# Optimization experiments

Hardware: AMD Instinct MI355X
Metric: run time of the kernel (lower is better)

## Reference

```python
import jax, jax.numpy as jnp
import numpy as np

IN_F, OUT_F, R = 4096, 4096, 16
SCALING = 32.0 / R  # lora_alpha / r


def setup_inputs() -> dict:
    key = jax.random.key(0)
    kx, kw, kb, ka, kB = jax.random.split(key, 5)
    bound_w = 1.0 / np.sqrt(IN_F)  # kaiming_uniform a=sqrt(5) on (out,in) -> U(-1/sqrt(in), 1/sqrt(in))
    x = jax.random.normal(kx, (4, 4096, IN_F), dtype=jnp.float32)
    weight = jax.random.uniform(kw, (OUT_F, IN_F), jnp.float32, -bound_w, bound_w)
    bias = jax.random.uniform(kb, (OUT_F,), jnp.float32, -bound_w, bound_w)
    lora_A = jax.random.uniform(ka, (R, IN_F), jnp.float32, -bound_w, bound_w)
    # B is zero-init in the module; use small random values so the LoRA path is exercised
    lora_B = jax.random.normal(kB, (OUT_F, R), dtype=jnp.float32) * 0.01
    return {"x": x, "weight": weight, "bias": bias, "lora_A": lora_A, "lora_B": lora_B}


def reference(x, weight, bias, lora_A, lora_B):
    # base: F.linear(x, W, b) = x @ W.T + b
    base_out = jnp.einsum("bsi,oi->bso", x, weight) + bias
    # low-rank path: (x @ A.T) @ B.T * scaling  (dropout=0 -> identity)
    xr = jnp.einsum("bsi,ri->bsr", x, lora_A)  # [b, s, r]
    lora_out = jnp.einsum("bsr,or->bso", xr, lora_B) * SCALING
    return base_out + lora_out
```

## Files before the change

### kernel.cpp

```cpp
#include <hip/hip_runtime.h>
#include <hip/hip_bf16.h>


typedef __attribute__((ext_vector_type(8))) short bf16x8;
typedef __attribute__((ext_vector_type(16))) float f32x16;
typedef __attribute__((ext_vector_type(4))) unsigned short u16x4;

#define M_DIM 16384
#define N_DIM 4096
#define K_DIM 4096
#define NT 64

__device__ __forceinline__ unsigned short f2bf(float f) {
    unsigned int u = __builtin_bit_cast(unsigned int, f);
    unsigned int r = u + 0x7FFFu + ((u >> 16) & 1u);
    return (unsigned short)(r >> 16);
}

__device__ __forceinline__ void async16(const void* g, void* l) {
    __builtin_amdgcn_global_load_lds(
        (const __attribute__((address_space(1))) unsigned int*)g,
        (__attribute__((address_space(3))) unsigned int*)l,
        16, 0, 0);
}

__global__ void __launch_bounds__(256) cast_x_kernel(
    const float* __restrict__ x, unsigned short* __restrict__ y) {
    const int total = 512 * 256 * 64;
    int idx = blockIdx.x * 256 + threadIdx.x;
    const int stride = gridDim.x * 256;
    for (; idx < total; idx += stride) {
        const int frag = idx >> 6, l = idx & 63;
        const int m = ((frag >> 8) << 5) + (l & 31);
        const int k = ((frag & 255) << 4) + ((l >> 5) << 3);
        const float4* px = reinterpret_cast<const float4*>(&x[(size_t)m * K_DIM + k]);
        float4 a = px[0], b = px[1];
        unsigned short r[8] = { f2bf(a.x), f2bf(a.y), f2bf(a.z), f2bf(a.w),
                                f2bf(b.x), f2bf(b.y), f2bf(b.z), f2bf(b.w) };
        *reinterpret_cast<bf16x8*>(&y[((size_t)frag << 9) + (l << 3)]) =
            *reinterpret_cast<const bf16x8*>(r);
    }
}

__global__ void __launch_bounds__(256) weff_kernel(
    const float* __restrict__ W, const float* __restrict__ lA,
    const float* __restrict__ lB, unsigned short* __restrict__ out) {
    constexpr int K = K_DIM, R = 16;
    constexpr float S = 2.0f;
    int o = blockIdx.x;
    int t = threadIdx.x;
    float b[R];
#pragma unroll
    for (int r = 0; r < R; ++r) b[r] = lB[o * R + r];
#pragma unroll
    for (int c = 0; c < 4; ++c) {
        int i = c * 1024 + t * 4;
        float4 wv = *reinterpret_cast<const float4*>(&W[o * K + i]);
        float sx = 0.f, sy = 0.f, sz = 0.f, sw = 0.f;
#pragma unroll
        for (int r = 0; r < R; ++r) {
            float4 a = *reinterpret_cast<const float4*>(&lA[r * K + i]);
            sx += b[r] * a.x; sy += b[r] * a.y;
            sz += b[r] * a.z; sw += b[r] * a.w;
        }
        u16x4 ov = { f2bf(wv.x + S * sx), f2bf(wv.y + S * sy),
                     f2bf(wv.z + S * sz), f2bf(wv.w + S * sw) };
        const int frag = (o >> 5) * 256 + (i >> 4);
        const int lane_ = (o & 31) + (((i >> 3) & 1) << 5);
        *reinterpret_cast<u16x4*>(
            &out[((size_t)frag << 9) + (lane_ << 3) + (i & 7)]) = ov;
    }
}

#define ASTAGE(t, bsel, jlo, jhi)                                             \
    _Pragma("unroll") for (int j = (jlo); j <= (jhi); ++j) {                  \
        const int g = wid * 4 + j;                                            \
        async16(A + (((size_t)(bm * 8 + (g >> 2)) * 256 + (t) * 4 + (g & 3))  \
                     << 9) + (lane << 3),                                     \
                lds + (bsel) * 65536 + g * 1024 + (lane << 4));               \
    }

#define BSTAGE(t, bsel)                                                       \
    _Pragma("unroll") for (int j = 0; j < 4; ++j) {                           \
        const int g = wid * 4 + j;                                            \
        async16(B + (((size_t)(bn * 8 + (g >> 2)) * 256 + (t) * 4 + (g & 3))  \
                     << 9) + (lane << 3),                                     \
                lds + (bsel) * 65536 + 32768 + g * 1024 + (lane << 4));       \
    }

#define LDA32(dst, mh, kh, bsel)                                              \
    _Pragma("unroll") for (int mm = 0; mm < 2; ++mm)                          \
    _Pragma("unroll") for (int kk = 0; kk < 2; ++kk)                          \
        dst[mm * 2 + kk] = *(const bf16x8*)(lds + (bsel) * 65536 +            \
            (((wm * 4 + (mh) * 2 + mm) * 4 + (kh) * 2 + kk) << 10) +          \
            (lane << 4));

#define LDB32(dst, kh, bsel)                                                  \
    _Pragma("unroll") for (int nn = 0; nn < 2; ++nn)                          \
    _Pragma("unroll") for (int kk = 0; kk < 2; ++kk)                          \
        dst[nn * 2 + kk] = *(const bf16x8*)(lds + (bsel) * 65536 + 32768 +    \
            (((wn * 2 + nn) * 4 + (kh) * 2 + kk) << 10) + (lane << 4));

#define MMQ(asrc, bsrc, mh)                                                   \
    __builtin_amdgcn_s_setprio(1);                                            \
    _Pragma("unroll") for (int kk = 0; kk < 2; ++kk)                          \
    _Pragma("unroll") for (int mm = 0; mm < 2; ++mm)                          \
    _Pragma("unroll") for (int nn = 0; nn < 2; ++nn)                          \
        acc[(mh) * 2 + mm][nn] = __builtin_amdgcn_mfma_f32_32x32x16_bf16(     \
            asrc[mm * 2 + kk], bsrc[nn * 2 + kk], acc[(mh) * 2 + mm][nn],     \
            0, 0, 0);                                                         \
    __builtin_amdgcn_s_setprio(0)

#define CFENCE() asm volatile("" ::: "memory")
#define WAIT_LGKM(n)                                                          \
    asm volatile("s_waitcnt lgkmcnt(" #n ")" ::: "memory");                   \
    __builtin_amdgcn_sched_barrier(0)

#define KTILE(t)                                                              \
    {                                                                         \
        const int bs_ = (t) & 1, bo_ = bs_ ^ 1;                               \
        LDA32(arE, 0, 0, bs_);                                    \
        LDB32(br0, 0, bs_);                                       \
        if ((t) + 1 < NT) ASTAGE((t) + 1, bo_, 0, 1);                         \
        LDA32(arO, 1, 0, bs_);                                     \
        WAIT_LGKM(4);                                                         \
        MMQ(arE, br0, 0);                                                     \
        if ((t) + 1 < NT) ASTAGE((t) + 1, bo_, 2, 3);                         \
        LDA32(arE2, 0, 1, bs_);                                   \
        LDB32(br1, 1, bs_);                                       \
        WAIT_LGKM(8);                                                         \
        MMQ(arO, br0, 1);                                                     \
        LDA32(arO2, 1, 1, bs_);                                    \
        WAIT_LGKM(4);                                                         \
        MMQ(arE2, br1, 0);                                                    \
        CFENCE();                                                             \
        __builtin_amdgcn_s_barrier();      \
        CFENCE();                                                             \
        if ((t) + 2 < NT) BSTAGE((t) + 2, bs_);                               \
        WAIT_LGKM(0);                                                         \
        MMQ(arO2, br1, 1);                                                    \
        if ((t) < NT - 2) {                                                   \
            asm volatile("s_waitcnt vmcnt(4)" ::: "memory");                  \
        } else {                                                              \
            asm volatile("s_waitcnt vmcnt(0)" ::: "memory");                  \
        }                                                                     \
        __builtin_amdgcn_s_barrier();                                         \
        CFENCE();                                                             \
    }

__global__ void __launch_bounds__(512, 2) gemmfl_kernel(
    const unsigned short* __restrict__ A,
    const unsigned short* __restrict__ B,
    const float* __restrict__ bias,
    float* __restrict__ C) {
    __shared__ __align__(1024) char lds[131072];

    const int tid = threadIdx.x;
    const int lane = tid & 63, wid = tid >> 6;
    const int wm = wid >> 2, wn = wid & 3;
    const int lc = lane & 31, hi = lane >> 5;

    const int bid = blockIdx.x;
    const int swz = (bid & 7) * 128 + (bid >> 3);
    const int bm = swz >> 4, bn = swz & 15;

    f32x16 acc[4][2] = {};
    bf16x8 arE[4], arO[4], arE2[4], arO2[4], br0[4], br1[4];

    BSTAGE(0, 0);
    ASTAGE(0, 0, 0, 3);
    BSTAGE(1, 1);
    asm volatile("s_waitcnt vmcnt(4)" ::: "memory");
    __builtin_amdgcn_s_barrier();
    CFENCE();

#pragma unroll 2
    for (int t = 0; t < NT; ++t) {
        KTILE(t);
    }

    const int row0 = bm * 256 + wm * 128;
    const int col0 = bn * 256 + wn * 64;
#pragma unroll
    for (int n = 0; n < 2; ++n) {
        const int col = col0 + n * 32 + lc;
        const float bv = bias[col];
#pragma unroll
        for (int m = 0; m < 4; ++m) {
#pragma unroll
            for (int g = 0; g < 4; ++g) {
#pragma unroll
                for (int r = 0; r < 4; ++r) {
                    const int row = row0 + m * 32 + g * 8 + 4 * hi + r;
                    C[(size_t)row * N_DIM + col] = acc[m][n][g * 4 + r] + bv;
                }
            }
        }
    }
}

extern "C" void kernel_launch(void* const* d_in, const int* in_sizes, int n_in,
                              void* d_out, int out_size, void* d_ws, size_t ws_size,
                              hipStream_t stream) {
    const float* x    = (const float*)d_in[0];
    const float* W    = (const float*)d_in[1];
    const float* bias = (const float*)d_in[2];
    const float* lA   = (const float*)d_in[3];
    const float* lB   = (const float*)d_in[4];
    float* out = (float*)d_out;

    unsigned short* xb   = (unsigned short*)d_ws;
    unsigned short* weff = (unsigned short*)((char*)d_ws + 134217728);

    cast_x_kernel<<<4096, 256, 0, stream>>>(x, xb);
    weff_kernel<<<N_DIM, 256, 0, stream>>>(W, lA, lB, weff);
    gemmfl_kernel<<<(M_DIM / 256) * (N_DIM / 256), 512, 0, stream>>>(
        xb, weff, bias, out);
}
```

Before: 631.4 us.

## Restructure GEMM k-loop into barrier-separated phases with cross-tile fragment prefetch

Reorganizes the main bf16 MFMA k-tile loop into ping-pong style phases separated by workgroup barriers between each MFMA group and its LDS loads. The first A/B fragments of the next tile are now loaded at the end of the current tile, overlapping with the last MFMA group. The B-tile global-to-LDS prefetch is split into two halves issued in different phases. The aim is to interleave LDS reads, global loads and MFMA across waves more evenly. The cost is many extra s_barrier instructions per tile, which may add stalls.

```diff
diff --git a/kernel.cpp b/kernel.cpp
--- a/kernel.cpp
+++ b/kernel.cpp
@@ -80,8 +80,8 @@
                 lds + (bsel) * 65536 + g * 1024 + (lane << 4));               \
     }
 
-#define BSTAGE(t, bsel)                                                       \
-    _Pragma("unroll") for (int j = 0; j < 4; ++j) {                           \
+#define BSTAGE(t, bsel, jlo, jhi)                                             \
+    _Pragma("unroll") for (int j = (jlo); j <= (jhi); ++j) {                  \
         const int g = wid * 4 + j;                                            \
         async16(B + (((size_t)(bn * 8 + (g >> 2)) * 256 + (t) * 4 + (g & 3))  \
                      << 9) + (lane << 3),                                     \
@@ -112,6 +112,10 @@
     __builtin_amdgcn_s_setprio(0)
 
 #define CFENCE() asm volatile("" ::: "memory")
+#define BAR()                                                                 \
+    CFENCE();                                                                 \
+    __builtin_amdgcn_s_barrier();                                             \
+    CFENCE()
 #define WAIT_LGKM(n)                                                          \
     asm volatile("s_waitcnt lgkmcnt(" #n ")" ::: "memory");                   \
     __builtin_amdgcn_sched_barrier(0)
@@ -119,26 +123,30 @@
 #define KTILE(t)                                                              \
     {                                                                         \
         const int bs_ = (t) & 1, bo_ = bs_ ^ 1;                               \
-        LDA32(arE, 0, 0, bs_);                                    \
-        LDB32(br0, 0, bs_);                                       \
+                      \
         if ((t) + 1 < NT) ASTAGE((t) + 1, bo_, 0, 1);                         \
-        LDA32(arO, 1, 0, bs_);                                     \
+        LDA32(arO, 1, 0, bs_);                                                \
+        BAR();                                                                \
         WAIT_LGKM(4);                                                         \
         MMQ(arE, br0, 0);                                                     \
+        BAR();                                                                \
+                                          \
         if ((t) + 1 < NT) ASTAGE((t) + 1, bo_, 2, 3);                         \
-        LDA32(arE2, 0, 1, bs_);                                   \
-        LDB32(br1, 1, bs_);                                       \
+        LDA32(arE2, 0, 1, bs_);                                               \
+        LDB32(br1, 1, bs_);                                                   \
+        BAR();                                                                \
         WAIT_LGKM(8);                                                         \
         MMQ(arO, br0, 1);                                                     \
-        LDA32(arO2, 1, 1, bs_);                                    \
+        BAR();                                                                \
+                                          \
+        if ((t) + 2 < NT) BSTAGE((t) + 2, bs_, 0, 1);                         \
+        LDA32(arO2, 1, 1, bs_);                                               \
+        BAR();                                                                \
         WAIT_LGKM(4);                                                         \
         MMQ(arE2, br1, 0);                                                    \
-        CFENCE();                                                             \
-        __builtin_amdgcn_s_barrier();      \
-        CFENCE();                                                             \
-        if ((t) + 2 < NT) BSTAGE((t) + 2, bs_);                               \
-        WAIT_LGKM(0);                                                         \
-        MMQ(arO2, br1, 1);                                                    \
+        BAR();                                                                \
+                           \
+        if ((t) + 2 < NT) BSTAGE((t) + 2, bs_, 2, 3);                         \
         if ((t) < NT - 2) {                                                   \
             asm volatile("s_waitcnt vmcnt(4)" ::: "memory");                  \
         } else {                                                              \
@@ -146,9 +154,17 @@
         }                                                                     \
         __builtin_amdgcn_s_barrier();                                         \
         CFENCE();                                                             \
-    }
-
-__global__ void __launch_bounds__(512, 2) gemmfl_kernel(
+        if ((t) + 1 < NT) {                                                   \
+            LDA32(arE, 0, 0, bo_);                                            \
+            LDB32(br0, 0, bo_);                                               \
+            WAIT_LGKM(8);                                                     \
+        } else {                                                              \
+            WAIT_LGKM(0);                                                     \
+        }                                                                     \
+        MMQ(arO2, br1, 1);                                                    \
+    }
+
+__global__ void __launch_bounds__(512, 2) gemmph_kernel(
     const unsigned short* __restrict__ A,
     const unsigned short* __restrict__ B,
     const float* __restrict__ bias,
@@ -167,12 +183,14 @@
     f32x16 acc[4][2] = {};
     bf16x8 arE[4], arO[4], arE2[4], arO2[4], br0[4], br1[4];
 
-    BSTAGE(0, 0);
+    BSTAGE(0, 0, 0, 3);
     ASTAGE(0, 0, 0, 3);
-    BSTAGE(1, 1);
+    BSTAGE(1, 1, 0, 3);
     asm volatile("s_waitcnt vmcnt(4)" ::: "memory");
     __builtin_amdgcn_s_barrier();
     CFENCE();
+    LDA32(arE, 0, 0, 0);
+    LDB32(br0, 0, 0);
 
 #pragma unroll 2
     for (int t = 0; t < NT; ++t) {
@@ -214,6 +232,6 @@
 
     cast_x_kernel<<<4096, 256, 0, stream>>>(x, xb);
     weff_kernel<<<N_DIM, 256, 0, stream>>>(W, lA, lB, weff);
-    gemmfl_kernel<<<(M_DIM / 256) * (N_DIM / 256), 512, 0, stream>>>(
+    gemmph_kernel<<<(M_DIM / 256) * (N_DIM / 256), 512, 0, stream>>>(
         xb, weff, bias, out);
 }
```

Measured after the change: 635.5 us. About the same (+0.6%).

## Double waves per block with smaller per-wave tiles and a simpler prefetch pipeline

Applied to the files above, without the earlier changes.

The GEMM block grows from 512 to 1024 threads. Each wave now computes a 64x64 sub-tile instead of 128x64, which roughly halves accumulator and fragment registers. The finely interleaved LDS-wait schedule is replaced by a plain double buffer: prefetch the next K tile, run two MFMA half-steps, then wait and barrier. The goal is more waves to hide latency, at the cost of a lower MFMA-to-LDS-read ratio per wave and less overlap inside each tile. LDS use stays at 128KB per block, so the requested four blocks per CU cannot actually be resident.

```diff
diff --git a/kernel.cpp b/kernel.cpp
--- a/kernel.cpp
+++ b/kernel.cpp
@@ -72,83 +72,66 @@
     }
 }
 
-#define ASTAGE(t, bsel, jlo, jhi)                                             \
-    _Pragma("unroll") for (int j = (jlo); j <= (jhi); ++j) {                  \
-        const int g = wid * 4 + j;                                            \
+#define ASTAGE(t, bsel)                                                       \
+    _Pragma("unroll") for (int j = 0; j < 2; ++j) {                           \
+        const int g = wid * 2 + j;                                            \
         async16(A + (((size_t)(bm * 8 + (g >> 2)) * 256 + (t) * 4 + (g & 3))  \
                      << 9) + (lane << 3),                                     \
                 lds + (bsel) * 65536 + g * 1024 + (lane << 4));               \
     }
 
 #define BSTAGE(t, bsel)                                                       \
-    _Pragma("unroll") for (int j = 0; j < 4; ++j) {                           \
-        const int g = wid * 4 + j;                                            \
+    _Pragma("unroll") for (int j = 0; j < 2; ++j) {                           \
+        const int g = wid * 2 + j;                                            \
         async16(B + (((size_t)(bn * 8 + (g >> 2)) * 256 + (t) * 4 + (g & 3))  \
                      << 9) + (lane << 3),                                     \
                 lds + (bsel) * 65536 + 32768 + g * 1024 + (lane << 4));       \
     }
 
-#define LDA32(dst, mh, kh, bsel)                                              \
+#define LDA32(kh, bsel)                                                       \
     _Pragma("unroll") for (int mm = 0; mm < 2; ++mm)                          \
     _Pragma("unroll") for (int kk = 0; kk < 2; ++kk)                          \
-        dst[mm * 2 + kk] = *(const bf16x8*)(lds + (bsel) * 65536 +            \
-            (((wm * 4 + (mh) * 2 + mm) * 4 + (kh) * 2 + kk) << 10) +          \
-            (lane << 4));
-
-#define LDB32(dst, kh, bsel)                                                  \
+        ar[mm * 2 + kk] = *(const bf16x8*)(lds + (bsel) * 65536 +             \
+            (((wm * 2 + mm) * 4 + (kh) * 2 + kk) << 10) + (lane << 4));
+
+#define LDB32(kh, bsel)                                                       \
     _Pragma("unroll") for (int nn = 0; nn < 2; ++nn)                          \
     _Pragma("unroll") for (int kk = 0; kk < 2; ++kk)                          \
-        dst[nn * 2 + kk] = *(const bf16x8*)(lds + (bsel) * 65536 + 32768 +    \
+        br[nn * 2 + kk] = *(const bf16x8*)(lds + (bsel) * 65536 + 32768 +     \
             (((wn * 2 + nn) * 4 + (kh) * 2 + kk) << 10) + (lane << 4));
 
-#define MMQ(asrc, bsrc, mh)                                                   \
+#define MMH()                                                                 \
     __builtin_amdgcn_s_setprio(1);                                            \
     _Pragma("unroll") for (int kk = 0; kk < 2; ++kk)                          \
     _Pragma("unroll") for (int mm = 0; mm < 2; ++mm)                          \
     _Pragma("unroll") for (int nn = 0; nn < 2; ++nn)                          \
-        acc[(mh) * 2 + mm][nn] = __builtin_amdgcn_mfma_f32_32x32x16_bf16(     \
-            asrc[mm * 2 + kk], bsrc[nn * 2 + kk], acc[(mh) * 2 + mm][nn],     \
-            0, 0, 0);                                                         \
+        acc[mm][nn] = __builtin_amdgcn_mfma_f32_32x32x16_bf16(                \
+            ar[mm * 2 + kk], br[nn * 2 + kk], acc[mm][nn], 0, 0, 0);          \
     __builtin_amdgcn_s_setprio(0)
 
 #define CFENCE() asm volatile("" ::: "memory")
-#define WAIT_LGKM(n)                                                          \
-    asm volatile("s_waitcnt lgkmcnt(" #n ")" ::: "memory");                   \
-    __builtin_amdgcn_sched_barrier(0)
 
 #define KTILE(t)                                                              \
     {                                                                         \
         const int bs_ = (t) & 1, bo_ = bs_ ^ 1;                               \
-        LDA32(arE, 0, 0, bs_);                                    \
-        LDB32(br0, 0, bs_);                                       \
-        if ((t) + 1 < NT) ASTAGE((t) + 1, bo_, 0, 1);                         \
-        LDA32(arO, 1, 0, bs_);                                     \
-        WAIT_LGKM(4);                                                         \
-        MMQ(arE, br0, 0);                                                     \
-        if ((t) + 1 < NT) ASTAGE((t) + 1, bo_, 2, 3);                         \
-        LDA32(arE2, 0, 1, bs_);                                   \
-        LDB32(br1, 1, bs_);                                       \
-        WAIT_LGKM(8);                                                         \
-        MMQ(arO, br0, 1);                                                     \
-        LDA32(arO2, 1, 1, bs_);                                    \
-        WAIT_LGKM(4);                                                         \
-        MMQ(arE2, br1, 0);                                                    \
-        CFENCE();                                                             \
-        __builtin_amdgcn_s_barrier();      \
-        CFENCE();                                                             \
-        if ((t) + 2 < NT) BSTAGE((t) + 2, bs_);                               \
-        WAIT_LGKM(0);                                                         \
-        MMQ(arO2, br1, 1);                                                    \
-        if ((t) < NT - 2) {                                                   \
-            asm volatile("s_waitcnt vmcnt(4)" ::: "memory");                  \
-        } else {                                                              \
+        if ((t) + 1 < NT) {                                                   \
+            ASTAGE((t) + 1, bo_);                                             \
+            BSTAGE((t) + 1, bo_);                                             \
+        }                                                                     \
+        LDA32(0, bs_);                                                        \
+        LDB32(0, bs_);                                                        \
+        MMH();                                                                \
+        LDA32(1, bs_);                                                        \
+        LDB32(1, bs_);                                                        \
+        MMH();                                                                \
+        if ((t) + 1 < NT) {                                                   \
             asm volatile("s_waitcnt vmcnt(0)" ::: "memory");                  \
+            __builtin_amdgcn_s_barrier();                                     \
+            CFENCE();                                                         \
         }                                                                     \
-        __builtin_amdgcn_s_barrier();                                         \
-        CFENCE();                                                             \
-    }
-
-__global__ void __launch_bounds__(512, 2) gemmfl_kernel(
+    }
+
+__global__ void __launch_bounds__(1024, 4) gemmoc_kernel(
     const unsigned short* __restrict__ A,
     const unsigned short* __restrict__ B,
     const float* __restrict__ bias,
@@ -164,13 +147,12 @@
     const int swz = (bid & 7) * 128 + (bid >> 3);
     const int bm = swz >> 4, bn = swz & 15;
 
-    f32x16 acc[4][2] = {};
-    bf16x8 arE[4], arO[4], arE2[4], arO2[4], br0[4], br1[4];
-
+    f32x16 acc[2][2] = {};
+    bf16x8 ar[4], br[4];
+
+    ASTAGE(0, 0);
     BSTAGE(0, 0);
-    ASTAGE(0, 0, 0, 3);
-    BSTAGE(1, 1);
-    asm volatile("s_waitcnt vmcnt(4)" ::: "memory");
+    asm volatile("s_waitcnt vmcnt(0)" ::: "memory");
     __builtin_amdgcn_s_barrier();
     CFENCE();
 
@@ -179,14 +161,14 @@
         KTILE(t);
     }
 
-    const int row0 = bm * 256 + wm * 128;
+    const int row0 = bm * 256 + wm * 64;
     const int col0 = bn * 256 + wn * 64;
 #pragma unroll
     for (int n = 0; n < 2; ++n) {
         const int col = col0 + n * 32 + lc;
         const float bv = bias[col];
 #pragma unroll
-        for (int m = 0; m < 4; ++m) {
+        for (int m = 0; m < 2; ++m) {
 #pragma unroll
             for (int g = 0; g < 4; ++g) {
 #pragma unroll
@@ -214,6 +196,6 @@
 
     cast_x_kernel<<<4096, 256, 0, stream>>>(x, xb);
     weff_kernel<<<N_DIM, 256, 0, stream>>>(W, lA, lB, weff);
-    gemmfl_kernel<<<(M_DIM / 256) * (N_DIM / 256), 512, 0, stream>>>(
+    gemmoc_kernel<<<(M_DIM / 256) * (N_DIM / 256), 1024, 0, stream>>>(
         xb, weff, bias, out);
 }
```

Measured after the change: 658.3 us. 1.04x slower.
